# Performance work log

Measured on AMD Instinct MI355X. Metric: run time of the kernel, lower is better.

Reference implementation:

```python
import jax, jax.numpy as jnp
import numpy as np

V, D, DFF, E, K, L = 32000, 1024, 4096, 8, 2, 2
B, S = 2, 1024


def _layer_norm(x, scale, bias, eps=1e-5):
    mu = jnp.mean(x, axis=-1, keepdims=True)
    var = jnp.var(x, axis=-1, keepdims=True)
    return (x - mu) * jax.lax.rsqrt(var + eps) * scale + bias


def setup_inputs() -> dict:
    key = jax.random.key(0)
    ks = jax.random.split(key, 16)
    s = 0.02
    return {
        "input_ids": jax.random.randint(ks[0], (B, S), 0, V, dtype=jnp.int32),
        "emb": jax.random.normal(ks[1], (V, D), jnp.float32) * s,
        "t_ln_scale": jnp.ones((L, D), jnp.float32),
        "t_ln_bias": jnp.zeros((L, D), jnp.float32),
        "t_w1": jax.random.normal(ks[2], (L, D, DFF), jnp.float32) * s,
        "t_b1": jnp.zeros((L, DFF), jnp.float32),
        "t_w2": jax.random.normal(ks[3], (L, DFF, D), jnp.float32) * s,
        "t_b2": jnp.zeros((L, D), jnp.float32),
        "Wr": jax.random.normal(ks[4], (D, E), jnp.float32) * s,
        "br": jnp.zeros((E,), jnp.float32),
        "e_w1": jax.random.normal(ks[5], (E, D, DFF), jnp.float32) * s,
        "e_b1": jnp.zeros((E, DFF), jnp.float32),
        "e_w2": jax.random.normal(ks[6], (E, DFF, D), jnp.float32) * s,
        "e_b2": jnp.zeros((E, D), jnp.float32),
        "Wl": jax.random.normal(ks[7], (D, V), jnp.float32) * s,
        "bl": jnp.zeros((V,), jnp.float32),
    }


def reference(input_ids, emb, t_ln_scale, t_ln_bias, t_w1, t_b1, t_w2, t_b2,
              Wr, br, e_w1, e_b1, e_w2, e_b2, Wl, bl):
    # token embeddings: [B,S,D]
    x = emb[input_ids]

    # temporal abstraction: L pre-LN residual MLP blocks
    for l in range(L):
        h = _layer_norm(x, t_ln_scale[l], t_ln_bias[l])
        h = jax.nn.gelu(jnp.einsum('bsd,df->bsf', h, t_w1[l]) + t_b1[l])
        x = x + jnp.einsum('bsf,fd->bsd', h, t_w2[l]) + t_b2[l]

    # router: top-k renormalized softmax over experts, scattered to [B,S,E]
    r_logits = jnp.einsum('bsd,de->bse', x, Wr) + br
    top_vals, top_idx = jax.lax.top_k(r_logits, K)
    top_w = jax.nn.softmax(top_vals, axis=-1)
    routing_weights = jnp.put_along_axis(
        jnp.zeros_like(r_logits), top_idx, top_w, axis=-1, inplace=False)

    # dense all-experts stack: [B,S,E,D]
    h = jax.nn.gelu(jnp.einsum('bsd,edf->bsef', x, e_w1) + e_b1)
    expert_out = jnp.einsum('bsef,efd->bsed', h, e_w2) + e_b2

    # sparse-weighted combine
    y = jnp.einsum('bse,bsed->bsd', routing_weights, expert_out)

    logits = jnp.einsum('bsd,dv->bsv', y, Wl) + bl
    return logits, routing_weights
```

## Files before the change

### kernel.cpp

```cpp
#include <hip/hip_runtime.h>
#include <stdint.h>

typedef __bf16 bf16;
typedef __bf16 bf16x8 __attribute__((ext_vector_type(8)));
typedef __bf16 bf16x4 __attribute__((ext_vector_type(4)));
typedef float f32x4 __attribute__((ext_vector_type(4)));

#define DEV __device__ __forceinline__

static constexpr int Dm   = 1024;
static constexpr int DFFm = 4096;
static constexpr int Tm   = 2048;
static constexpr int Vm   = 32000;

#define GLOAD_LDS16(g, l)                                                      \
  __builtin_amdgcn_global_load_lds(                                            \
      (const __attribute__((address_space(1))) unsigned int*)(g),              \
      (__attribute__((address_space(3))) unsigned int*)(l), 16, 0, 0)

DEV float gelu_tanh(float v) {
  float u = 0.7978845608028654f * (v + 0.044715f * v * v * v);
  float e = __expf(2.0f * u);
  float t = 1.0f - 2.0f / (e + 1.0f);
  return 0.5f * v * (1.0f + t);
}

template <bool SWZ>
__launch_bounds__(512, 2)
__global__ void gemm256_8p(const bf16* __restrict__ A, const bf16* __restrict__ B,
                           const float* __restrict__ bias, float* __restrict__ out,
                           int Kc, int Nc) {
  __shared__ bf16 lds[65536];
  const int tid  = threadIdx.x;
  const int lane = tid & 63;
  const int wid  = tid >> 6;
  const int wr   = wid >> 2;
  const int wc   = wid & 3;

  int bx = blockIdx.x, by = blockIdx.y;
  if constexpr (SWZ) {
    const int gx = gridDim.x, gy = gridDim.y;
    const int nwg = gx * gy;
    const int lin = by * gx + bx;
    const int q = nwg >> 3, r = nwg & 7;
    const int xcd = lin & 7, loc = lin >> 3;
    const int nid = (xcd < r ? xcd * (q + 1) : r * (q + 1) + (xcd - r) * q) + loc;
    bx = nid / gy; by = nid % gy;
  }
  const long am0 = (long)by * 256;
  const long bn0 = (long)bx * 256;
  const long K = Kc;
  const int NT = Kc >> 6;

  const int sub = (lane & 7) ^ (lane >> 3);
  const int rw  = wid * 8 + (lane >> 3);
  const bf16 *aS[4], *bS[4];
#pragma unroll
  for (int j = 0; j < 4; ++j) {
    aS[j] = A + (am0 + j * 64 + rw) * K + sub * 8;
    bS[j] = B + (bn0 + j * 64 + rw) * K + sub * 8;
  }
  char* ldsc = (char*)(void*)lds;

#define STG_A(kt, j)                                                           \
  GLOAD_LDS16(aS[j] + (long)(kt) * 64,                                         \
              ldsc + ((kt) & 1) * 65536 + ((j) * 64 + wid * 8) * 128)
#define STG_B(kt, j)                                                           \
  GLOAD_LDS16(bS[j] + (long)(kt) * 64,                                         \
              ldsc + ((kt) & 1) * 65536 + 32768 + ((j) * 64 + wid * 8) * 128)

  STG_B(0, 0); STG_B(0, 1); STG_B(0, 2); STG_B(0, 3);
  STG_A(0, 0); STG_A(0, 2); STG_A(0, 1); STG_A(0, 3);
  if (NT > 1) {
    STG_B(1, 0); STG_B(1, 1); STG_B(1, 2); STG_B(1, 3);
    STG_A(1, 0); STG_A(1, 2);
    asm volatile("s_waitcnt vmcnt(6)" ::: "memory");
  } else {
    asm volatile("s_waitcnt vmcnt(0)" ::: "memory");
  }
  __builtin_amdgcn_s_barrier();

  f32x4 acc[8][4] = {};
  const int r15 = lane & 15;
  const int kcs = lane >> 4;
  const int x7  = lane & 7;
  const int q80 = (kcs ^ x7) << 3;
  const int q81 = ((kcs + 4) ^ x7) << 3;

  for (int t = 0; t < NT; ++t) {
    const bf16* LAb = lds + (t & 1) * 32768 + wr * 128 * 64;
    const bf16* LBb = lds + (t & 1) * 32768 + 16384 + wc * 64 * 64;
    bf16x8 b0[4], b1[4];

    {
      bf16x8 a0, a1, a2, a3;
#pragma unroll
      for (int n = 0; n < 4; ++n) {
        b0[n] = *(const bf16x8*)(LBb + (n * 16 + r15) * 64 + q80);
        b1[n] = *(const bf16x8*)(LBb + (n * 16 + r15) * 64 + q81);
      }
      a0 = *(const bf16x8*)(LAb + (0 * 16 + r15) * 64 + q80);
      a1 = *(const bf16x8*)(LAb + (0 * 16 + r15) * 64 + q81);
      a2 = *(const bf16x8*)(LAb + (1 * 16 + r15) * 64 + q80);
      a3 = *(const bf16x8*)(LAb + (1 * 16 + r15) * 64 + q81);
      if (t + 1 < NT) { STG_A(t + 1, 1); STG_A(t + 1, 3); }
      __builtin_amdgcn_s_barrier();
      asm volatile("s_waitcnt lgkmcnt(0)" ::: "memory");
      __builtin_amdgcn_s_setprio(1);
#pragma unroll
      for (int n = 0; n < 4; ++n) {
        acc[0][n] = __builtin_amdgcn_mfma_f32_16x16x32_bf16(a0, b0[n], acc[0][n], 0, 0, 0);
        acc[0][n] = __builtin_amdgcn_mfma_f32_16x16x32_bf16(a1, b1[n], acc[0][n], 0, 0, 0);
        acc[1][n] = __builtin_amdgcn_mfma_f32_16x16x32_bf16(a2, b0[n], acc[1][n], 0, 0, 0);
        acc[1][n] = __builtin_amdgcn_mfma_f32_16x16x32_bf16(a3, b1[n], acc[1][n], 0, 0, 0);
      }
      __builtin_amdgcn_s_setprio(0);
      __builtin_amdgcn_s_barrier();
    }
    {
      bf16x8 a0, a1, a2, a3;
      a0 = *(const bf16x8*)(LAb + (2 * 16 + r15) * 64 + q80);
      a1 = *(const bf16x8*)(LAb + (2 * 16 + r15) * 64 + q81);
      a2 = *(const bf16x8*)(LAb + (3 * 16 + r15) * 64 + q80);
      a3 = *(const bf16x8*)(LAb + (3 * 16 + r15) * 64 + q81);
      if (t + 2 < NT) { STG_B(t + 2, 0); STG_B(t + 2, 1); }
      __builtin_amdgcn_s_barrier();
      asm volatile("s_waitcnt lgkmcnt(0)" ::: "memory");
      __builtin_amdgcn_s_setprio(1);
#pragma unroll
      for (int n = 0; n < 4; ++n) {
        acc[2][n] = __builtin_amdgcn_mfma_f32_16x16x32_bf16(a0, b0[n], acc[2][n], 0, 0, 0);
        acc[2][n] = __builtin_amdgcn_mfma_f32_16x16x32_bf16(a1, b1[n], acc[2][n], 0, 0, 0);
        acc[3][n] = __builtin_amdgcn_mfma_f32_16x16x32_bf16(a2, b0[n], acc[3][n], 0, 0, 0);
        acc[3][n] = __builtin_amdgcn_mfma_f32_16x16x32_bf16(a3, b1[n], acc[3][n], 0, 0, 0);
      }
      __builtin_amdgcn_s_setprio(0);
      __builtin_amdgcn_s_barrier();
    }
    {
      bf16x8 a0, a1, a2, a3;
      a0 = *(const bf16x8*)(LAb + (4 * 16 + r15) * 64 + q80);
      a1 = *(const bf16x8*)(LAb + (4 * 16 + r15) * 64 + q81);
      a2 = *(const bf16x8*)(LAb + (5 * 16 + r15) * 64 + q80);
      a3 = *(const bf16x8*)(LAb + (5 * 16 + r15) * 64 + q81);
      if (t + 2 < NT) { STG_B(t + 2, 2); STG_B(t + 2, 3); }
      __builtin_amdgcn_s_barrier();
      asm volatile("s_waitcnt lgkmcnt(0)" ::: "memory");
      __builtin_amdgcn_s_setprio(1);
#pragma unroll
      for (int n = 0; n < 4; ++n) {
        acc[4][n] = __builtin_amdgcn_mfma_f32_16x16x32_bf16(a0, b0[n], acc[4][n], 0, 0, 0);
        acc[4][n] = __builtin_amdgcn_mfma_f32_16x16x32_bf16(a1, b1[n], acc[4][n], 0, 0, 0);
        acc[5][n] = __builtin_amdgcn_mfma_f32_16x16x32_bf16(a2, b0[n], acc[5][n], 0, 0, 0);
        acc[5][n] = __builtin_amdgcn_mfma_f32_16x16x32_bf16(a3, b1[n], acc[5][n], 0, 0, 0);
      }
      __builtin_amdgcn_s_setprio(0);
      __builtin_amdgcn_s_barrier();
    }
    {
      bf16x8 a0, a1, a2, a3;
      a0 = *(const bf16x8*)(LAb + (6 * 16 + r15) * 64 + q80);
      a1 = *(const bf16x8*)(LAb + (6 * 16 + r15) * 64 + q81);
      a2 = *(const bf16x8*)(LAb + (7 * 16 + r15) * 64 + q80);
      a3 = *(const bf16x8*)(LAb + (7 * 16 + r15) * 64 + q81);
      if (t + 2 < NT) {
        STG_A(t + 2, 0); STG_A(t + 2, 2);
        asm volatile("s_waitcnt vmcnt(6)" ::: "memory");
      } else if (t + 1 < NT) {
        asm volatile("s_waitcnt vmcnt(0)" ::: "memory");
      }
      __builtin_amdgcn_s_barrier();
      asm volatile("s_waitcnt lgkmcnt(0)" ::: "memory");
      __builtin_amdgcn_s_setprio(1);
#pragma unroll
      for (int n = 0; n < 4; ++n) {
        acc[6][n] = __builtin_amdgcn_mfma_f32_16x16x32_bf16(a0, b0[n], acc[6][n], 0, 0, 0);
        acc[6][n] = __builtin_amdgcn_mfma_f32_16x16x32_bf16(a1, b1[n], acc[6][n], 0, 0, 0);
        acc[7][n] = __builtin_amdgcn_mfma_f32_16x16x32_bf16(a2, b0[n], acc[7][n], 0, 0, 0);
        acc[7][n] = __builtin_amdgcn_mfma_f32_16x16x32_bf16(a3, b1[n], acc[7][n], 0, 0, 0);
      }
      __builtin_amdgcn_s_setprio(0);
      __builtin_amdgcn_s_barrier();
    }
  }
#undef STG_A
#undef STG_B

  const long N = Nc;
#pragma unroll
  for (int m = 0; m < 8; ++m) {
#pragma unroll
    for (int n = 0; n < 4; ++n) {
      const long col = bn0 + wc * 64 + n * 16 + r15;
      const float bv = bias[col];
#pragma unroll
      for (int r = 0; r < 4; ++r) {
        const long row = am0 + wr * 128 + m * 16 + (lane >> 4) * 4 + r;
        out[row * N + col] = acc[m][n][r] + bv;
      }
    }
  }
}

enum { EPI_GELU_SPLIT = 0, EPI_RESID = 1, EPI_GELU_BF16 = 2, EPI_MOE = 3 };

struct GemmP {
  const bf16* Ah;
  const bf16* Bh;
  const float* bias;
  const float* rwp;
  const int* cnt;
  const int* idx;
  float* outF;
  bf16* outH;
  int K; int N;
  int lda; int ldb; int ldo;
  long aBS, bBS, outBS;
  int biasBS;
  int ebase;
  int kcShift; int kcK;
  int aT, aS2, bT, bS2;
};

template <int EPI, bool GATHER, bool SWZ>
__launch_bounds__(256, 2)
__global__ void gemm_bt(GemmP p) {
  __shared__ bf16 lds[16384];
  bf16* ldsA = lds;
  bf16* ldsB = lds + 8192;

  const int tid  = threadIdx.x;
  const int lane = tid & 63;
  const int wid  = tid >> 6;
  const int wr   = wid >> 1;
  const int wc   = wid & 1;
  const int z    = blockIdx.z;
  const int kc   = z & ((1 << p.kcShift) - 1);
  const int ze   = z >> p.kcShift;

  int bx = blockIdx.x, by = blockIdx.y;
  if constexpr (SWZ) {
    const int gx = gridDim.x, gy = gridDim.y;
    const int nwg = gx * gy;
    const int lin = by * gx + bx;
    const int q = nwg >> 3, r = nwg & 7;
    const int xcd = lin & 7, loc = lin >> 3;
    const int nid = (xcd < r ? xcd * (q + 1) : r * (q + 1) + (xcd - r) * q) + loc;
    bx = nid / gy; by = nid % gy;
  }

  const long am0 = (long)by * 128;
  const long bn0 = (long)bx * 128;

  int cntE = 0;
  const int* il = nullptr;
  if constexpr (GATHER || EPI == EPI_MOE) {
    cntE = p.cnt[p.ebase + ze];
    if (am0 >= cntE) return;
    il = p.idx + (long)(p.ebase + ze) * 2048;
  }

  const long lda = p.lda, ldb = p.ldb;
  const long K = p.K;
  const long kco = (long)kc * p.kcK;

  const int sub = (lane & 7) ^ (lane >> 3);
  const int rIn = wid * 8 + (lane >> 3);

  const bf16 *aS[4], *bS[4];
  {
    const bf16* Bb = p.Bh + (long)ze * p.bBS + bn0 * ldb;
    const bf16* Ab = p.Ah + (long)ze * p.aBS + am0 * lda;
#pragma unroll
    for (int j = 0; j < 4; ++j) {
      const int row = j * 32 + rIn;
      bS[j] = Bb + (long)row * ldb + sub * 8;
      if constexpr (GATHER) {
        const int rt = (int)am0 + row;
        const long grow = il[rt < cntE ? rt : 0];
        aS[j] = p.Ah + grow * lda + sub * 8;
      } else {
        aS[j] = Ab + (long)row * lda + sub * 8;
      }
    }
  }
  char* dstA[4];
#pragma unroll
  for (int j = 0; j < 4; ++j)
    dstA[j] = (char*)(void*)lds + (j * 256 + wid * 64) * 16;

  f32x4 acc[4][4] = {};

  const int r15 = lane & 15;
  const int kcs = lane >> 4;
  const int xk  = lane & 7;

  for (long k0 = 0; k0 < K; k0 += 64) {
    const long kv = kco + k0;
    const long ka = (kv >= p.aT) ? kv - p.aS2 : kv;
    const long kb = (kv >= p.bT) ? kv - p.bS2 : kv;
    __syncthreads();
#pragma unroll
    for (int j = 0; j < 4; ++j) {
      GLOAD_LDS16(aS[j] + ka, dstA[j]);
      GLOAD_LDS16(bS[j] + kb, dstA[j] + 16384);
    }
    __syncthreads();
#pragma unroll
    for (int h = 0; h < 2; ++h) {
      const int q8 = ((kcs + 4 * h) ^ xk) << 3;
      bf16x8 a[4], b[4];
#pragma unroll
      for (int m = 0; m < 4; ++m)
        a[m] = *(const bf16x8*)(ldsA + (wr * 64 + m * 16 + r15) * 64 + q8);
#pragma unroll
      for (int n = 0; n < 4; ++n)
        b[n] = *(const bf16x8*)(ldsB + (wc * 64 + n * 16 + r15) * 64 + q8);
#pragma unroll
      for (int m = 0; m < 4; ++m)
#pragma unroll
        for (int n = 0; n < 4; ++n)
          acc[m][n] = __builtin_amdgcn_mfma_f32_16x16x32_bf16(a[m], b[n], acc[m][n], 0, 0, 0);
    }
  }

  const long N = p.N;
#pragma unroll
  for (int m = 0; m < 4; ++m) {
#pragma unroll
    for (int n = 0; n < 4; ++n) {
      const long col = bn0 + wc * 64 + n * 16 + (lane & 15);
      const float bv = (kc == 0) ? p.bias[(long)ze * p.biasBS + col] : 0.0f;
#pragma unroll
      for (int r = 0; r < 4; ++r) {
        const long row = am0 + wr * 64 + m * 16 + (lane >> 4) * 4 + r;
        float v = acc[m][n][r] + bv;
        if constexpr (EPI == EPI_GELU_SPLIT) {
          float g = gelu_tanh(v);
          bf16 hh = (bf16)g;
          long o = row * (long)p.ldo + col;
          p.outH[o] = hh;
          p.outH[o + N] = (bf16)(g - (float)hh);
        } else if constexpr (EPI == EPI_RESID) {
          atomicAdd(p.outF + row * N + col, v);
        } else if constexpr (EPI == EPI_GELU_BF16) {
          long o = (long)ze * p.outBS + row * N + col;
          p.outH[o] = (bf16)gelu_tanh(v);
        } else if constexpr (EPI == EPI_MOE) {
          if (row < cntE) {
            const int tok = il[row];
            const float wgt = p.rwp[(long)tok * 8 + p.ebase + ze];
            atomicAdd(p.outF + (long)tok * N + col, wgt * v);
          }
        }
      }
    }
  }
}

template <bool AUG>
__global__ void transpose_cvt(const float* __restrict__ in, bf16* __restrict__ out,
                              int R, int C, long inBS, long outBS) {
  __shared__ float tile[64][65];
  const float* inp = in + (long)blockIdx.z * inBS;
  const long c0 = (long)blockIdx.x * 64;
  const long r0 = (long)blockIdx.y * 64;
  const int tx = threadIdx.x;
  const int ty = threadIdx.y;
#pragma unroll
  for (int i = 0; i < 4; ++i) {
    const int r = ty + i * 16;
    const float4 v = *(const float4*)(inp + (r0 + r) * (long)C + c0 + tx * 4);
    tile[r][tx * 4 + 0] = v.x;
    tile[r][tx * 4 + 1] = v.y;
    tile[r][tx * 4 + 2] = v.z;
    tile[r][tx * 4 + 3] = v.w;
  }
  __syncthreads();
  const long ob = (long)blockIdx.z * outBS;
  const long stride = AUG ? 2L * R : (long)R;
#pragma unroll
  for (int j = 0; j < 4; ++j) {
    const int c = j * 16 + ty;
    bf16x4 h, l;
#pragma unroll
    for (int u = 0; u < 4; ++u) {
      float v = tile[tx * 4 + u][c];
      bf16 hh = (bf16)v;
      h[u] = hh;
      if constexpr (AUG) l[u] = (bf16)(v - (float)hh);
    }
    const long o = ob + (c0 + c) * stride + r0 + tx * 4;
    *(bf16x4*)(out + o) = h;
    if constexpr (AUG) *(bf16x4*)(out + o + R) = l;
  }
}

__global__ void embed_kernel(const int* __restrict__ ids, const float* __restrict__ emb,
                             float* __restrict__ x) {
  const long t = blockIdx.x;
  const int id = ids[t];
  ((float4*)(x + t * 1024))[threadIdx.x] = ((const float4*)(emb + (long)id * 1024))[threadIdx.x];
}

__global__ void ln_aug2_kernel(const float* __restrict__ x, const float* __restrict__ sc,
                               const float* __restrict__ bi, bf16* __restrict__ oa) {
  const long t = blockIdx.x;
  const int tid = threadIdx.x;
  const int lane = tid & 63, wid = tid >> 6;
  float4 a = ((const float4*)(x + t * 1024))[tid];
  float s = a.x + a.y + a.z + a.w;
  float q = a.x * a.x + a.y * a.y + a.z * a.z + a.w * a.w;
#pragma unroll
  for (int off = 32; off; off >>= 1) {
    s += __shfl_down(s, off);
    q += __shfl_down(q, off);
  }
  __shared__ float sr[4], qr[4];
  if (lane == 0) { sr[wid] = s; qr[wid] = q; }
  __syncthreads();
  s = sr[0] + sr[1] + sr[2] + sr[3];
  q = qr[0] + qr[1] + qr[2] + qr[3];
  const float mu = s * (1.0f / 1024.0f);
  const float var = q * (1.0f / 1024.0f) - mu * mu;
  const float rs = rsqrtf(var + 1e-5f);
#pragma unroll
  for (int j = 0; j < 4; ++j) {
    const int d = tid * 4 + j;
    const float g = (((const float*)&a)[j] - mu) * rs * sc[d] + bi[d];
    const bf16 h = (bf16)g;
    oa[t * 2048 + d] = h;
    oa[t * 2048 + 1024 + d] = (bf16)(g - (float)h);
  }
}

__global__ void router_kernel(const float* __restrict__ x, const float* __restrict__ Wr,
                              const float* __restrict__ br, float* __restrict__ rwo,
                              bf16* __restrict__ xb, int* __restrict__ cnt,
                              int* __restrict__ idx) {
  const long t = blockIdx.x;
  const int lane = threadIdx.x;
  float acc[8];
#pragma unroll
  for (int e = 0; e < 8; ++e) acc[e] = 0.0f;
  const float4* xr = (const float4*)(x + t * 1024);
#pragma unroll
  for (int j = 0; j < 4; ++j) {
    const int d4 = j * 64 + lane;
    float4 xv = xr[d4];
    bf16x4 xh;
    xh[0] = (bf16)xv.x; xh[1] = (bf16)xv.y; xh[2] = (bf16)xv.z; xh[3] = (bf16)xv.w;
    *(bf16x4*)(xb + t * 1024 + (long)d4 * 4) = xh;
#pragma unroll
    for (int u = 0; u < 4; ++u) {
      const float xs = ((const float*)&xv)[u];
      const float4* wp = (const float4*)(Wr + (long)(d4 * 4 + u) * 8);
      float4 w0 = wp[0], w1 = wp[1];
      acc[0] += xs * w0.x; acc[1] += xs * w0.y; acc[2] += xs * w0.z; acc[3] += xs * w0.w;
      acc[4] += xs * w1.x; acc[5] += xs * w1.y; acc[6] += xs * w1.z; acc[7] += xs * w1.w;
    }
  }
#pragma unroll
  for (int off = 32; off; off >>= 1)
#pragma unroll
    for (int e = 0; e < 8; ++e) acc[e] += __shfl_down(acc[e], off);
  if (lane == 0) {
    float v[8];
#pragma unroll
    for (int e = 0; e < 8; ++e) v[e] = acc[e] + br[e];
    int i0 = 0; float v0 = v[0];
    for (int e = 1; e < 8; ++e) if (v[e] > v0) { v0 = v[e]; i0 = e; }
    int i1 = -1; float v1 = -3.4e38f;
    for (int e = 0; e < 8; ++e) if (e != i0 && v[e] > v1) { v1 = v[e]; i1 = e; }
    float e1 = expf(v1 - v0);
    float den = 1.0f + e1;
    float w0 = 1.0f / den, w1 = e1 / den;
    float* o = rwo + t * 8;
#pragma unroll
    for (int e = 0; e < 8; ++e) o[e] = (e == i0) ? w0 : (e == i1 ? w1 : 0.0f);
    int p0 = atomicAdd(&cnt[i0], 1);
    idx[i0 * 2048 + p0] = (int)t;
    int p1 = atomicAdd(&cnt[i1], 1);
    idx[i1 * 2048 + p1] = (int)t;
  }
}

__global__ void cvt_bf16_kernel(const float* __restrict__ in, bf16* __restrict__ out, long n) {
  long i = ((long)blockIdx.x * blockDim.x + threadIdx.x) * 8;
  if (i >= n) return;
  float4 a = *(const float4*)(in + i);
  float4 b = *(const float4*)(in + i + 4);
  bf16x8 o;
  o[0] = (bf16)a.x; o[1] = (bf16)a.y; o[2] = (bf16)a.z; o[3] = (bf16)a.w;
  o[4] = (bf16)b.x; o[5] = (bf16)b.y; o[6] = (bf16)b.z; o[7] = (bf16)b.w;
  *(bf16x8*)(out + i) = o;
}

extern "C" void kernel_launch(void* const* d_in, const int* in_sizes, int n_in,
                              void* d_out, int out_size, void* d_ws, size_t ws_size,
                              hipStream_t stream) {
  (void)in_sizes; (void)n_in; (void)out_size; (void)ws_size;
  const int*   ids  = (const int*)d_in[0];
  const float* emb  = (const float*)d_in[1];
  const float* tlns = (const float*)d_in[2];
  const float* tlnb = (const float*)d_in[3];
  const float* tw1  = (const float*)d_in[4];
  const float* tb1  = (const float*)d_in[5];
  const float* tw2  = (const float*)d_in[6];
  const float* tb2  = (const float*)d_in[7];
  const float* Wr   = (const float*)d_in[8];
  const float* br   = (const float*)d_in[9];
  const float* ew1  = (const float*)d_in[10];
  const float* eb1  = (const float*)d_in[11];
  const float* ew2  = (const float*)d_in[12];
  const float* eb2  = (const float*)d_in[13];
  const float* Wl   = (const float*)d_in[14];
  const float* bl   = (const float*)d_in[15];

  float* logits = (float*)d_out;
  float* rwout  = (float*)d_out + (long)Tm * Vm;

  size_t off = 0;
  auto take = [&](size_t bytes) {
    void* pp = (char*)d_ws + off;
    off += (bytes + 255) & ~(size_t)255;
    return pp;
  };
  float* X    = (float*)take((size_t)Tm * Dm * 4);
  bf16*  XB   = (bf16*) take((size_t)Tm * Dm * 2);
  float* Y    = (float*)take((size_t)Tm * Dm * 4);
  bf16*  YB   = (bf16*) take((size_t)Tm * Dm * 2);
  int*   cnt  = (int*)  take(8 * 4);
  int*   idxl = (int*)  take((size_t)8 * Tm * 4);
  char*  S    = (char*) take(134217728);

  bf16* A1  = (bf16*)S;
  bf16* W1A = (bf16*)(S + 8388608);
  bf16* W2A = (bf16*)(S + 25165824);
  bf16* HTA = (bf16*)(S + 41943040);
  bf16* EW1T = (bf16*)S;
  bf16* HE   = (bf16*)(S + 33554432);
  bf16* EW2T = (bf16*)(S + 100663296);
  bf16* WLT  = (bf16*)S;

  embed_kernel<<<dim3(Tm), dim3(256), 0, stream>>>(ids, emb, X);

  for (int l = 0; l < 2; ++l) {
    transpose_cvt<true><<<dim3(DFFm / 64, Dm / 64, 1), dim3(16, 16), 0, stream>>>(
        tw1 + (long)l * Dm * DFFm, W1A, Dm, DFFm, 0, 0);
    transpose_cvt<true><<<dim3(Dm / 64, DFFm / 64, 1), dim3(16, 16), 0, stream>>>(
        tw2 + (long)l * DFFm * Dm, W2A, DFFm, Dm, 0, 0);
    ln_aug2_kernel<<<dim3(Tm), dim3(256), 0, stream>>>(X, tlns + l * Dm, tlnb + l * Dm, A1);

    GemmP p1{};
    p1.Ah = A1; p1.Bh = W1A;
    p1.bias = tb1 + (long)l * DFFm;
    p1.outH = HTA;
    p1.K = 3072; p1.N = DFFm; p1.lda = 2048; p1.ldb = 2048; p1.ldo = 2 * DFFm;
    p1.aT = 2048; p1.aS2 = 2048; p1.bT = 1024; p1.bS2 = 1024;
    gemm_bt<EPI_GELU_SPLIT, false, true>
        <<<dim3(DFFm / 128, Tm / 128, 1), dim3(256), 0, stream>>>(p1);

    GemmP p2{};
    p2.Ah = HTA; p2.Bh = W2A;
    p2.bias = tb2 + (long)l * Dm;
    p2.outF = X;
    p2.K = 1536; p2.N = Dm; p2.lda = 8192; p2.ldb = 8192;
    p2.kcShift = 3; p2.kcK = 1536;
    p2.aT = 8192; p2.aS2 = 8192; p2.bT = 4096; p2.bS2 = 4096;
    gemm_bt<EPI_RESID, false, true>
        <<<dim3(Dm / 128, Tm / 128, 8), dim3(256), 0, stream>>>(p2);
  }

  hipMemsetAsync(cnt, 0, 8 * 4, stream);
  router_kernel<<<dim3(Tm), dim3(64), 0, stream>>>(X, Wr, br, rwout, XB, cnt, idxl);
  hipMemsetAsync(Y, 0, (size_t)Tm * Dm * 4, stream);

  for (int q = 0; q < 2; ++q) {
    transpose_cvt<false><<<dim3(DFFm / 64, Dm / 64, 4), dim3(16, 16), 0, stream>>>(
        ew1 + (long)q * 4 * Dm * DFFm, EW1T, Dm, DFFm, (long)Dm * DFFm, (long)DFFm * Dm);
    transpose_cvt<false><<<dim3(Dm / 64, DFFm / 64, 4), dim3(16, 16), 0, stream>>>(
        ew2 + (long)q * 4 * DFFm * Dm, EW2T, DFFm, Dm, (long)DFFm * Dm, (long)Dm * DFFm);

    GemmP pe1{};
    pe1.Ah = XB; pe1.Bh = EW1T;
    pe1.bias = eb1 + (long)q * 4 * DFFm; pe1.biasBS = DFFm;
    pe1.outH = HE; pe1.outBS = (long)Tm * DFFm;
    pe1.aBS = 0; pe1.bBS = (long)DFFm * Dm;
    pe1.cnt = cnt; pe1.idx = idxl; pe1.ebase = q * 4;
    pe1.K = Dm; pe1.N = DFFm; pe1.lda = Dm; pe1.ldb = Dm;
    gemm_bt<EPI_GELU_BF16, true, true>
        <<<dim3(DFFm / 128, Tm / 128, 4), dim3(256), 0, stream>>>(pe1);

    GemmP pe2{};
    pe2.Ah = HE; pe2.aBS = (long)Tm * DFFm;
    pe2.Bh = EW2T; pe2.bBS = (long)Dm * DFFm;
    pe2.bias = eb2 + (long)q * 4 * Dm; pe2.biasBS = Dm;
    pe2.rwp = rwout; pe2.cnt = cnt; pe2.idx = idxl; pe2.ebase = q * 4;
    pe2.outF = Y;
    pe2.K = 1024; pe2.N = Dm; pe2.lda = DFFm; pe2.ldb = DFFm;
    pe2.kcShift = 2; pe2.kcK = 1024;
    gemm_bt<EPI_MOE, false, true>
        <<<dim3(Dm / 128, Tm / 128, 16), dim3(256), 0, stream>>>(pe2);
  }

  cvt_bf16_kernel<<<dim3(Tm * Dm / (256 * 8)), dim3(256), 0, stream>>>(Y, YB, (long)Tm * Dm);
  transpose_cvt<false><<<dim3(Vm / 64, Dm / 64, 1), dim3(16, 16), 0, stream>>>(
      Wl, WLT, Dm, Vm, 0, 0);
  gemm256_8p<true><<<dim3(Vm / 256, Tm / 256, 1), dim3(512), 0, stream>>>(
      YB, WLT, bl, logits, Dm, Vm);
}
```

Baseline: 978.3 us.

## Run temporal MLP in plain bf16, recompute near-tie router tokens in split precision

The two temporal MLP layers now run with single bf16 operands (K=1024 instead of the hi/lo augmented K=3072/1536) for all tokens. The router then flags tokens whose 2nd/3rd expert logit margin is under a tolerance, and only those rows are recomputed through the augmented-precision path, then scattered back and rerouted. This cuts most of the split-precision GEMM work in the temporal blocks. It risks mismatched logits when the reduced precision shifts the residual stream beyond tolerance on non-flagged tokens, and it adds several small kernels plus an extra buffer copy.

```diff
diff --git a/kernel.cpp b/kernel.cpp
--- a/kernel.cpp
+++ b/kernel.cpp
@@ -12,6 +12,7 @@
 static constexpr int DFFm = 4096;
 static constexpr int Tm   = 2048;
 static constexpr int Vm   = 32000;
+static constexpr float TAU = 0.04f;
 
 #define GLOAD_LDS16(g, l)                                                      \
   __builtin_amdgcn_global_load_lds(                                            \
@@ -252,12 +253,14 @@
   const long am0 = (long)by * 128;
   const long bn0 = (long)bx * 128;
 
-  int cntE = 0;
+  int cntE = 1 << 30;
   const int* il = nullptr;
   if constexpr (GATHER || EPI == EPI_MOE) {
     cntE = p.cnt[p.ebase + ze];
     if (am0 >= cntE) return;
     il = p.idx + (long)(p.ebase + ze) * 2048;
+  } else {
+    if (p.cnt) { cntE = p.cnt[0]; if (am0 >= cntE) return; }
   }
 
   const long lda = p.lda, ldb = p.ldb;
@@ -336,13 +339,15 @@
         const long row = am0 + wr * 64 + m * 16 + (lane >> 4) * 4 + r;
         float v = acc[m][n][r] + bv;
         if constexpr (EPI == EPI_GELU_SPLIT) {
-          float g = gelu_tanh(v);
-          bf16 hh = (bf16)g;
-          long o = row * (long)p.ldo + col;
-          p.outH[o] = hh;
-          p.outH[o + N] = (bf16)(g - (float)hh);
+          if (row < cntE) {
+            float g = gelu_tanh(v);
+            bf16 hh = (bf16)g;
+            long o = row * (long)p.ldo + col;
+            p.outH[o] = hh;
+            p.outH[o + N] = (bf16)(g - (float)hh);
+          }
         } else if constexpr (EPI == EPI_RESID) {
-          atomicAdd(p.outF + row * N + col, v);
+          if (row < cntE) atomicAdd(p.outF + row * N + col, v);
         } else if constexpr (EPI == EPI_GELU_BF16) {
           long o = (long)ze * p.outBS + row * N + col;
           p.outH[o] = (bf16)gelu_tanh(v);
@@ -403,12 +408,9 @@
   ((float4*)(x + t * 1024))[threadIdx.x] = ((const float4*)(emb + (long)id * 1024))[threadIdx.x];
 }
 
-__global__ void ln_aug2_kernel(const float* __restrict__ x, const float* __restrict__ sc,
-                               const float* __restrict__ bi, bf16* __restrict__ oa) {
-  const long t = blockIdx.x;
-  const int tid = threadIdx.x;
-  const int lane = tid & 63, wid = tid >> 6;
-  float4 a = ((const float4*)(x + t * 1024))[tid];
+DEV void ln_row(const float* xrow, float4& a, float& mu, float& rs,
+                const int tid, const int lane, const int wid) {
+  a = ((const float4*)xrow)[tid];
   float s = a.x + a.y + a.z + a.w;
   float q = a.x * a.x + a.y * a.y + a.z * a.z + a.w * a.w;
 #pragma unroll
@@ -421,23 +423,48 @@
   __syncthreads();
   s = sr[0] + sr[1] + sr[2] + sr[3];
   q = qr[0] + qr[1] + qr[2] + qr[3];
-  const float mu = s * (1.0f / 1024.0f);
+  mu = s * (1.0f / 1024.0f);
   const float var = q * (1.0f / 1024.0f) - mu * mu;
-  const float rs = rsqrtf(var + 1e-5f);
+  rs = rsqrtf(var + 1e-5f);
+}
+
+__global__ void ln_bf16_kernel(const float* __restrict__ x, const float* __restrict__ sc,
+                               const float* __restrict__ bi, bf16* __restrict__ oh) {
+  const long t = blockIdx.x;
+  const int tid = threadIdx.x, lane = tid & 63, wid = tid >> 6;
+  float4 a; float mu, rs;
+  ln_row(x + t * 1024, a, mu, rs, tid, lane, wid);
+  bf16x4 h;
+#pragma unroll
+  for (int j = 0; j < 4; ++j) {
+    const int d = tid * 4 + j;
+    h[j] = (bf16)((((const float*)&a)[j] - mu) * rs * sc[d] + bi[d]);
+  }
+  *(bf16x4*)(oh + t * 1024 + tid * 4) = h;
+}
+
+__global__ void ln_aug2c_kernel(const float* __restrict__ xc, const float* __restrict__ sc,
+                                const float* __restrict__ bi, bf16* __restrict__ oa,
+                                const int* __restrict__ fcnt) {
+  const long b = blockIdx.x;
+  if ((int)b >= *fcnt) return;
+  const int tid = threadIdx.x, lane = tid & 63, wid = tid >> 6;
+  float4 a; float mu, rs;
+  ln_row(xc + b * 1024, a, mu, rs, tid, lane, wid);
 #pragma unroll
   for (int j = 0; j < 4; ++j) {
     const int d = tid * 4 + j;
     const float g = (((const float*)&a)[j] - mu) * rs * sc[d] + bi[d];
     const bf16 h = (bf16)g;
-    oa[t * 2048 + d] = h;
-    oa[t * 2048 + 1024 + d] = (bf16)(g - (float)h);
+    oa[b * 2048 + d] = h;
+    oa[b * 2048 + 1024 + d] = (bf16)(g - (float)h);
   }
 }
 
 __global__ void router_kernel(const float* __restrict__ x, const float* __restrict__ Wr,
                               const float* __restrict__ br, float* __restrict__ rwo,
-                              bf16* __restrict__ xb, int* __restrict__ cnt,
-                              int* __restrict__ idx) {
+                              bf16* __restrict__ xb, int* __restrict__ top2,
+                              int* __restrict__ fcnt, int* __restrict__ fidx) {
   const long t = blockIdx.x;
   const int lane = threadIdx.x;
   float acc[8];
@@ -455,6 +482,58 @@
     for (int u = 0; u < 4; ++u) {
       const float xs = ((const float*)&xv)[u];
       const float4* wp = (const float4*)(Wr + (long)(d4 * 4 + u) * 8);
+      float4 w0 = wp[0], w1 = wp[1];
+      acc[0] += xs * w0.x; acc[1] += xs * w0.y; acc[2] += xs * w0.z; acc[3] += xs * w0.w;
+      acc[4] += xs * w1.x; acc[5] += xs * w1.y; acc[6] += xs * w1.z; acc[7] += xs * w1.w;
+    }
+  }
+#pragma unroll
+  for (int off = 32; off; off >>= 1)
+#pragma unroll
+    for (int e = 0; e < 8; ++e) acc[e] += __shfl_down(acc[e], off);
+  if (lane == 0) {
+    float v[8];
+#pragma unroll
+    for (int e = 0; e < 8; ++e) v[e] = acc[e] + br[e];
+    int i0 = 0; float v0 = v[0];
+    for (int e = 1; e < 8; ++e) if (v[e] > v0) { v0 = v[e]; i0 = e; }
+    int i1 = -1; float v1 = -3.4e38f;
+    for (int e = 0; e < 8; ++e) if (e != i0 && v[e] > v1) { v1 = v[e]; i1 = e; }
+    float m3 = -3.4e38f;
+    for (int e = 0; e < 8; ++e) if (e != i0 && e != i1 && v[e] > m3) m3 = v[e];
+    float e1 = expf(v1 - v0);
+    float den = 1.0f + e1;
+    float w0 = 1.0f / den, w1 = e1 / den;
+    float* o = rwo + t * 8;
+#pragma unroll
+    for (int e = 0; e < 8; ++e) o[e] = (e == i0) ? w0 : (e == i1 ? w1 : 0.0f);
+    top2[t] = i0 | (i1 << 8);
+    if (v1 - m3 < TAU) {
+      int pp = atomicAdd(fcnt, 1);
+      fidx[pp] = (int)t;
+    }
+  }
+}
+
+__global__ void router2_kernel(const float* __restrict__ x, const float* __restrict__ Wr,
+                               const float* __restrict__ br, float* __restrict__ rwo,
+                               int* __restrict__ top2, const int* __restrict__ fcnt,
+                               const int* __restrict__ fidx) {
+  const int b = blockIdx.x;
+  if (b >= *fcnt) return;
+  const long t = fidx[b];
+  const int lane = threadIdx.x;
+  float acc[8];
+#pragma unroll
+  for (int e = 0; e < 8; ++e) acc[e] = 0.0f;
+  const float4* xr = (const float4*)(x + t * 1024);
+#pragma unroll
+  for (int j = 0; j < 4; ++j) {
+    float4 xv = xr[j * 64 + lane];
+#pragma unroll
+    for (int u = 0; u < 4; ++u) {
+      const float xs = ((const float*)&xv)[u];
+      const float4* wp = (const float4*)(Wr + (long)((j * 64 + lane) * 4 + u) * 8);
       float4 w0 = wp[0], w1 = wp[1];
       acc[0] += xs * w0.x; acc[1] += xs * w0.y; acc[2] += xs * w0.z; acc[3] += xs * w0.w;
       acc[4] += xs * w1.x; acc[5] += xs * w1.y; acc[6] += xs * w1.z; acc[7] += xs * w1.w;
@@ -478,11 +557,41 @@
     float* o = rwo + t * 8;
 #pragma unroll
     for (int e = 0; e < 8; ++e) o[e] = (e == i0) ? w0 : (e == i1 ? w1 : 0.0f);
-    int p0 = atomicAdd(&cnt[i0], 1);
-    idx[i0 * 2048 + p0] = (int)t;
-    int p1 = atomicAdd(&cnt[i1], 1);
-    idx[i1 * 2048 + p1] = (int)t;
-  }
+    top2[t] = i0 | (i1 << 8);
+  }
+}
+
+__global__ void build_lists(const int* __restrict__ top2, int* __restrict__ cnt,
+                            int* __restrict__ idx) {
+  const int t = blockIdx.x * 256 + threadIdx.x;
+  const int rec = top2[t];
+  const int e0 = rec & 255, e1 = (rec >> 8) & 255;
+  int p0 = atomicAdd(&cnt[e0], 1);
+  idx[e0 * 2048 + p0] = t;
+  int p1 = atomicAdd(&cnt[e1], 1);
+  idx[e1 * 2048 + p1] = t;
+}
+
+__global__ void gather_rows(const float* __restrict__ x0, const int* __restrict__ fidx,
+                            const int* __restrict__ fcnt, float* __restrict__ xc) {
+  const int b = blockIdx.x;
+  if (b >= *fcnt) return;
+  const long t = fidx[b];
+  ((float4*)(xc + (long)b * 1024))[threadIdx.x] =
+      ((const float4*)(x0 + t * 1024))[threadIdx.x];
+}
+
+__global__ void scatter_rows(const float* __restrict__ xc, const int* __restrict__ fidx,
+                             const int* __restrict__ fcnt, float* __restrict__ x,
+                             bf16* __restrict__ xb) {
+  const int b = blockIdx.x;
+  if (b >= *fcnt) return;
+  const long t = fidx[b];
+  float4 v = ((const float4*)(xc + (long)b * 1024))[threadIdx.x];
+  ((float4*)(x + t * 1024))[threadIdx.x] = v;
+  bf16x4 h;
+  h[0] = (bf16)v.x; h[1] = (bf16)v.y; h[2] = (bf16)v.z; h[3] = (bf16)v.w;
+  *(bf16x4*)(xb + t * 1024 + (long)threadIdx.x * 4) = h;
 }
 
 __global__ void cvt_bf16_kernel(const float* __restrict__ in, bf16* __restrict__ out, long n) {
@@ -526,54 +635,90 @@
     off += (bytes + 255) & ~(size_t)255;
     return pp;
   };
+  float* X0   = (float*)take((size_t)Tm * Dm * 4);
   float* X    = (float*)take((size_t)Tm * Dm * 4);
   bf16*  XB   = (bf16*) take((size_t)Tm * Dm * 2);
   float* Y    = (float*)take((size_t)Tm * Dm * 4);
   bf16*  YB   = (bf16*) take((size_t)Tm * Dm * 2);
+  float* XC   = (float*)take((size_t)Tm * Dm * 4);
+  int*   top2 = (int*)  take((size_t)Tm * 4);
   int*   cnt  = (int*)  take(8 * 4);
+  int*   fcnt = (int*)  take(256);
+  int*   fidx = (int*)  take((size_t)Tm * 4);
   int*   idxl = (int*)  take((size_t)8 * Tm * 4);
   char*  S    = (char*) take(134217728);
 
-  bf16* A1  = (bf16*)S;
-  bf16* W1A = (bf16*)(S + 8388608);
-  bf16* W2A = (bf16*)(S + 25165824);
-  bf16* HTA = (bf16*)(S + 41943040);
+  bf16* W1A = (bf16*)S;
+  bf16* W2A = (bf16*)(S + 33554432);
+  bf16* A1  = (bf16*)(S + 67108864);
+  bf16* HT  = (bf16*)(S + 75497472);
+  const long W1S = 4096L * 2048, W2S = 1024L * 8192;
   bf16* EW1T = (bf16*)S;
   bf16* HE   = (bf16*)(S + 33554432);
   bf16* EW2T = (bf16*)(S + 100663296);
   bf16* WLT  = (bf16*)S;
 
-  embed_kernel<<<dim3(Tm), dim3(256), 0, stream>>>(ids, emb, X);
+  embed_kernel<<<dim3(Tm), dim3(256), 0, stream>>>(ids, emb, X0);
+  hipMemcpyAsync(X, X0, (size_t)Tm * Dm * 4, hipMemcpyDeviceToDevice, stream);
 
   for (int l = 0; l < 2; ++l) {
     transpose_cvt<true><<<dim3(DFFm / 64, Dm / 64, 1), dim3(16, 16), 0, stream>>>(
-        tw1 + (long)l * Dm * DFFm, W1A, Dm, DFFm, 0, 0);
+        tw1 + (long)l * Dm * DFFm, W1A + l * W1S, Dm, DFFm, 0, 0);
     transpose_cvt<true><<<dim3(Dm / 64, DFFm / 64, 1), dim3(16, 16), 0, stream>>>(
-        tw2 + (long)l * DFFm * Dm, W2A, DFFm, Dm, 0, 0);
-    ln_aug2_kernel<<<dim3(Tm), dim3(256), 0, stream>>>(X, tlns + l * Dm, tlnb + l * Dm, A1);
-
-    GemmP p1{};
-    p1.Ah = A1; p1.Bh = W1A;
-    p1.bias = tb1 + (long)l * DFFm;
-    p1.outH = HTA;
-    p1.K = 3072; p1.N = DFFm; p1.lda = 2048; p1.ldb = 2048; p1.ldo = 2 * DFFm;
-    p1.aT = 2048; p1.aS2 = 2048; p1.bT = 1024; p1.bS2 = 1024;
+        tw2 + (long)l * DFFm * Dm, W2A + l * W2S, DFFm, Dm, 0, 0);
+    ln_bf16_kernel<<<dim3(Tm), dim3(256), 0, stream>>>(X, tlns + l * Dm, tlnb + l * Dm, A1);
+
+    GemmP f1{};
+    f1.Ah = A1; f1.Bh = W1A + l * W1S;
+    f1.bias = tb1 + (long)l * DFFm;
+    f1.outH = HT;
+    f1.K = Dm; f1.N = DFFm; f1.lda = Dm; f1.ldb = 2048;
+    gemm_bt<EPI_GELU_BF16, false, true>
+        <<<dim3(DFFm / 128, Tm / 128, 1), dim3(256), 0, stream>>>(f1);
+
+    GemmP f2{};
+    f2.Ah = HT; f2.Bh = W2A + l * W2S;
+    f2.bias = tb2 + (long)l * Dm;
+    f2.outF = X;
+    f2.K = 1024; f2.N = Dm; f2.lda = DFFm; f2.ldb = 8192;
+    f2.kcShift = 2; f2.kcK = 1024;
+    gemm_bt<EPI_RESID, false, true>
+        <<<dim3(Dm / 128, Tm / 128, 4), dim3(256), 0, stream>>>(f2);
+  }
+
+  hipMemsetAsync(fcnt, 0, 4, stream);
+  router_kernel<<<dim3(Tm), dim3(64), 0, stream>>>(X, Wr, br, rwout, XB, top2, fcnt, fidx);
+
+  gather_rows<<<dim3(Tm), dim3(256), 0, stream>>>(X0, fidx, fcnt, XC);
+  for (int l = 0; l < 2; ++l) {
+    ln_aug2c_kernel<<<dim3(Tm), dim3(256), 0, stream>>>(XC, tlns + l * Dm,
+                                                        tlnb + l * Dm, A1, fcnt);
+    GemmP c1{};
+    c1.Ah = A1; c1.Bh = W1A + l * W1S;
+    c1.bias = tb1 + (long)l * DFFm;
+    c1.outH = HT;
+    c1.K = 3072; c1.N = DFFm; c1.lda = 2048; c1.ldb = 2048; c1.ldo = 2 * DFFm;
+    c1.aT = 2048; c1.aS2 = 2048; c1.bT = 1024; c1.bS2 = 1024;
+    c1.cnt = fcnt;
     gemm_bt<EPI_GELU_SPLIT, false, true>
-        <<<dim3(DFFm / 128, Tm / 128, 1), dim3(256), 0, stream>>>(p1);
-
-    GemmP p2{};
-    p2.Ah = HTA; p2.Bh = W2A;
-    p2.bias = tb2 + (long)l * Dm;
-    p2.outF = X;
-    p2.K = 1536; p2.N = Dm; p2.lda = 8192; p2.ldb = 8192;
-    p2.kcShift = 3; p2.kcK = 1536;
-    p2.aT = 8192; p2.aS2 = 8192; p2.bT = 4096; p2.bS2 = 4096;
+        <<<dim3(DFFm / 128, Tm / 128, 1), dim3(256), 0, stream>>>(c1);
+
+    GemmP c2{};
+    c2.Ah = HT; c2.Bh = W2A + l * W2S;
+    c2.bias = tb2 + (long)l * Dm;
+    c2.outF = XC;
+    c2.K = 1536; c2.N = Dm; c2.lda = 8192; c2.ldb = 8192;
+    c2.kcShift = 3; c2.kcK = 1536;
+    c2.aT = 8192; c2.aS2 = 8192; c2.bT = 4096; c2.bS2 = 4096;
+    c2.cnt = fcnt;
     gemm_bt<EPI_RESID, false, true>
-        <<<dim3(Dm / 128, Tm / 128, 8), dim3(256), 0, stream>>>(p2);
-  }
+        <<<dim3(Dm / 128, Tm / 128, 8), dim3(256), 0, stream>>>(c2);
+  }
+  scatter_rows<<<dim3(Tm), dim3(256), 0, stream>>>(XC, fidx, fcnt, X, XB);
+  router2_kernel<<<dim3(Tm), dim3(64), 0, stream>>>(X, Wr, br, rwout, top2, fcnt, fidx);
 
   hipMemsetAsync(cnt, 0, 8 * 4, stream);
-  router_kernel<<<dim3(Tm), dim3(64), 0, stream>>>(X, Wr, br, rwout, XB, cnt, idxl);
+  build_lists<<<dim3(Tm / 256), dim3(256), 0, stream>>>(top2, cnt, idxl);
   hipMemsetAsync(Y, 0, (size_t)Tm * Dm * 4, stream);
 
   for (int q = 0; q < 2; ++q) {
```

Result: slower. 1.110 ms (+13.5%).
